# Performance work log

Measured on AMD Instinct MI355X. Metric: run time of the kernel, lower is better.

The kernel has to match this reference:

```python
import jax, jax.numpy as jnp
import numpy as np

N_NODES = 100000
N_EDGES = 1600000
NUM_GRAPHS = 128


def _gcn_layer(x, W, b, senders, receivers, n_node):
    # Linear transform first (cheaper: feature dim small)
    x = x @ W + b  # [N, out]
    ones = jnp.ones(senders.shape[0], dtype=x.dtype)
    deg_s = jax.ops.segment_sum(ones, senders, n_node)     # out-degree
    deg_r = jax.ops.segment_sum(ones, receivers, n_node)   # in-degree
    # symmetric normalization: D^-1/2 A D^-1/2
    x = x * jax.lax.rsqrt(jnp.maximum(deg_s, 1.0))[:, None]
    x = jax.ops.segment_sum(x[senders], receivers, n_node)  # gather-scatter aggregation
    x = x * jax.lax.rsqrt(jnp.maximum(deg_r, 1.0))[:, None]
    return x


def setup_inputs() -> dict:
    key = jax.random.key(0)
    ks = jax.random.split(key, 10)
    x = jax.random.normal(ks[0], (N_NODES, 9), dtype=jnp.float32)
    senders = jax.random.randint(ks[1], (N_EDGES,), 0, N_NODES)
    receivers = jax.random.randint(ks[2], (N_EDGES,), 0, N_NODES)
    batch = jnp.sort(jax.random.randint(ks[3], (N_NODES,), 0, NUM_GRAPHS))
    # learned params (Dense: W [in,out], b [out]) with LeCun-normal-ish scale
    def dense(k, din, dout):
        return jax.random.normal(k, (din, dout), dtype=jnp.float32) / np.sqrt(din)
    W1 = dense(ks[4], 9, 64)
    b1 = jnp.zeros((64,), jnp.float32)
    W2 = dense(ks[5], 64, 128)
    b2 = jnp.zeros((128,), jnp.float32)
    W3 = dense(ks[6], 128, 2)
    b3 = jnp.zeros((2,), jnp.float32)
    return {"x": x, "senders": senders, "receivers": receivers, "batch": batch,
            "num_graphs": NUM_GRAPHS, "W1": W1, "b1": b1, "W2": W2, "b2": b2,
            "W3": W3, "b3": b3}


def reference(x, senders, receivers, batch, num_graphs, W1, b1, W2, b2, W3, b3):
    n_node = x.shape[0]
    x = jax.nn.relu(_gcn_layer(x, W1, b1, senders, receivers, n_node))
    x = jax.nn.relu(_gcn_layer(x, W2, b2, senders, receivers, n_node))
    x = _gcn_layer(x, W3, b3, senders, receivers, n_node)
    # graph-level pooling
    return jax.ops.segment_sum(x, batch, num_graphs)
```

## Files before the change

kernel.cpp:

```cpp
#include <hip/hip_runtime.h>
#include <hip/hip_bf16.h>
#include <cstddef>

#define NBMAX 512
#define BCAP 5120
#define BKCHUNK 3200

typedef unsigned short bf16t;
typedef __attribute__((ext_vector_type(8))) short short8;
typedef __attribute__((ext_vector_type(4))) float f32x4;

static __device__ __forceinline__ float2 up2(unsigned u) {
    return make_float2(__uint_as_float(u << 16), __uint_as_float(u & 0xffff0000u));
}
static __device__ __forceinline__ bf16t f2bf(float f) {
    unsigned u = __float_as_uint(f);
    u += 0x7fffu + ((u >> 16) & 1u);
    return (bf16t)(u >> 16);
}
static __device__ __forceinline__ unsigned pk2(float a, float b) {
    return (unsigned)f2bf(a) | ((unsigned)f2bf(b) << 16);
}

__global__ void k_bucket(const int* __restrict__ S, const int* __restrict__ R,
                         unsigned* __restrict__ bufR, unsigned char* __restrict__ bufS,
                         int* __restrict__ gCntR, int* __restrict__ gCntS,
                         const float* __restrict__ W2, bf16t* __restrict__ W2f,
                         int nE, int nB) {
    __shared__ int histR[NBMAX], lstR[NBMAX], baseR[NBMAX];
    __shared__ int histS[NBMAX], lstS[NBMAX], baseS[NBMAX];
    __shared__ int sm[256];
    __shared__ unsigned sortedR[BKCHUNK];
    __shared__ unsigned short bOfR[BKCHUNK];
    __shared__ unsigned char sortedS[BKCHUNK];
    __shared__ unsigned short bOfS[BKCHUNK];
    int t = threadIdx.x;
    int nSort = gridDim.x - 4;
    if (blockIdx.x >= nSort) {
        int tt = (blockIdx.x - nSort) * blockDim.x + t;
        if (tt < 1024) {
            int nt = tt >> 7, kh = (tt >> 6) & 1, lane = tt & 63;
            int n = nt * 16 + (lane & 15);
            int k0 = kh * 32 + (lane >> 4) * 8;
            uint4 p;
            p.x = pk2(W2[(k0 + 0) * 128 + n], W2[(k0 + 1) * 128 + n]);
            p.y = pk2(W2[(k0 + 2) * 128 + n], W2[(k0 + 3) * 128 + n]);
            p.z = pk2(W2[(k0 + 4) * 128 + n], W2[(k0 + 5) * 128 + n]);
            p.w = pk2(W2[(k0 + 6) * 128 + n], W2[(k0 + 7) * 128 + n]);
            ((uint4*)W2f)[tt] = p;
        }
        return;
    }
    for (int i = t; i < NBMAX; i += 256) { histR[i] = 0; histS[i] = 0; }
    __syncthreads();
    int chunk = (nE + nSort - 1) / nSort;
    int e0 = blockIdx.x * chunk;
    int e1 = min(e0 + chunk, nE);
    for (int e = e0 + t; e < e1; e += 256) {
        atomicAdd(&histR[R[e] >> 8], 1);
        atomicAdd(&histS[S[e] >> 8], 1);
    }
    __syncthreads();
    {
        int c0 = histR[2 * t], c1 = histR[2 * t + 1];
        int ps = c0 + c1;
        sm[t] = ps;
        __syncthreads();
        for (int off = 1; off < 256; off <<= 1) {
            int y = (t >= off) ? sm[t - off] : 0;
            __syncthreads();
            sm[t] += y;
            __syncthreads();
        }
        int ex = sm[t] - ps;
        lstR[2 * t] = ex;
        lstR[2 * t + 1] = ex + c0;
    }
    __syncthreads();
    {
        int c0 = histS[2 * t], c1 = histS[2 * t + 1];
        int ps = c0 + c1;
        sm[t] = ps;
        __syncthreads();
        for (int off = 1; off < 256; off <<= 1) {
            int y = (t >= off) ? sm[t - off] : 0;
            __syncthreads();
            sm[t] += y;
            __syncthreads();
        }
        int ex = sm[t] - ps;
        lstS[2 * t] = ex;
        lstS[2 * t + 1] = ex + c0;
    }
    __syncthreads();
    for (int i = t; i < nB; i += 256) {
        int cR = histR[i];
        baseR[i] = cR ? atomicAdd(&gCntR[i], cR) : 0;
        int cS = histS[i];
        baseS[i] = cS ? atomicAdd(&gCntS[i], cS) : 0;
    }
    for (int i = t; i < NBMAX; i += 256) { histR[i] = 0; histS[i] = 0; }
    __syncthreads();
    for (int e = e0 + t; e < e1; e += 256) {
        int r = R[e], s = S[e];
        int br = r >> 8;
        int p = lstR[br] + atomicAdd(&histR[br], 1);
        sortedR[p] = ((unsigned)(r & 255) << 24) | (unsigned)s;
        bOfR[p] = (unsigned short)br;
        int bs = s >> 8;
        int p2 = lstS[bs] + atomicAdd(&histS[bs], 1);
        sortedS[p2] = (unsigned char)(s & 255);
        bOfS[p2] = (unsigned short)bs;
    }
    __syncthreads();
    int cnt = e1 - e0;
    for (int i = t; i < cnt; i += 256) {
        int b = bOfR[i];
        int slot = baseR[b] + (i - lstR[b]);
        if (slot < BCAP) bufR[(size_t)b * BCAP + slot] = sortedR[i];
        int b2 = bOfS[i];
        int slot2 = baseS[b2] + (i - lstS[b2]);
        if (slot2 < BCAP) bufS[(size_t)b2 * BCAP + slot2] = sortedS[i];
    }
}

__global__ void k_pass2(const unsigned* __restrict__ bufR, const unsigned char* __restrict__ bufS,
                        const int* __restrict__ gCntR, const int* __restrict__ gCntS,
                        const float* __restrict__ x,
                        int* __restrict__ csr, int* __restrict__ cur, int* __restrict__ degR,
                        float* __restrict__ inv_r, float* __restrict__ inv_s,
                        bf16t* __restrict__ xs, int nN, int nB) {
    __shared__ int hist[256], incl[256], curs[256], histS[256];
    __shared__ int sm[256];
    __shared__ int gex[NBMAX];
    int t = threadIdx.x;
    int b = blockIdx.x;
    {
        int c0 = (2 * t < nB) ? gCntR[2 * t] : 0;
        int c1 = (2 * t + 1 < nB) ? gCntR[2 * t + 1] : 0;
        int ps = c0 + c1;
        sm[t] = ps;
        __syncthreads();
        for (int off = 1; off < 256; off <<= 1) {
            int y = (t >= off) ? sm[t - off] : 0;
            __syncthreads();
            sm[t] += y;
            __syncthreads();
        }
        int ex = sm[t] - ps;
        gex[2 * t] = ex;
        gex[2 * t + 1] = ex + c0;
    }
    hist[t] = 0; curs[t] = 0; histS[t] = 0;
    __syncthreads();
    int gb = gex[b];
    int cnt = gCntR[b];
    const unsigned* buf = bufR + (size_t)b * BCAP;
    for (int i = t; i < cnt; i += 256) atomicAdd(&hist[buf[i] >> 24], 1);
    __syncthreads();
    int v = hist[t];
    sm[t] = v;
    __syncthreads();
    for (int off = 1; off < 256; off <<= 1) {
        int y = (t >= off) ? sm[t - off] : 0;
        __syncthreads();
        sm[t] += y;
        __syncthreads();
    }
    incl[t] = sm[t];
    __syncthreads();
    int n0 = b << 8;
    int n = n0 + t;
    if (n < nN) {
        degR[n] = v;
        cur[n] = gb + incl[t];
        inv_r[n] = rsqrtf(fmaxf((float)v, 1.f));
    }
    for (int i = t; i < cnt; i += 256) {
        unsigned p = buf[i];
        int rl = p >> 24;
        int s = p & 0xFFFFFF;
        int pos = gb + (incl[rl] - hist[rl]) + atomicAdd(&curs[rl], 1);
        csr[pos] = s;
    }
    int cntS = gCntS[b];
    const unsigned char* bufs = bufS + (size_t)b * BCAP;
    for (int i = t; i < cntS; i += 256) atomicAdd(&histS[bufs[i]], 1);
    __syncthreads();
    if (n < nN) {
        float is = rsqrtf(fmaxf((float)histS[t], 1.f));
        inv_s[n] = is;
        float w[9];
#pragma unroll
        for (int k = 0; k < 9; k++) w[k] = x[(size_t)n * 9 + k] * is;
        uint4 pa, pb;
        pa.x = pk2(w[0], w[1]); pa.y = pk2(w[2], w[3]);
        pa.z = pk2(w[4], w[5]); pa.w = pk2(w[6], w[7]);
        pb.x = pk2(w[8], is);   pb.y = 0; pb.z = 0; pb.w = 0;
        uint4* o = (uint4*)(xs + (size_t)n * 16);
        o[0] = pa;
        o[1] = pb;
    }
}

__global__ void k_h1f(const unsigned* __restrict__ xs32, const float* __restrict__ W1,
                      const float* __restrict__ b1,
                      const int* __restrict__ csr, const int* __restrict__ cur,
                      const int* __restrict__ degR, const float* __restrict__ inv_r,
                      const float* __restrict__ inv_s,
                      bf16t* __restrict__ h1s, float* __restrict__ warr, int nN) {
    __shared__ float Wl[9 * 64];
    __shared__ float bl[64];
    for (int i = threadIdx.x; i < 9 * 64; i += blockDim.x) Wl[i] = W1[i];
    if (threadIdx.x < 64) bl[threadIdx.x] = b1[threadIdx.x];
    __syncthreads();
    int lane = threadIdx.x & 63;
    int wave = threadIdx.x >> 6;
    int n = blockIdx.x * 16 + wave * 4 + (lane >> 4);
    int ql = lane & 15;
    int g = ql >> 2;
    int f2 = ql & 3;
    int nc = min(n, nN - 1);
    int deg = degR[nc];
    int st = cur[nc] - deg;
    float4 A0 = {0.f, 0.f, 0.f, 0.f}, A1 = A0, A2 = A0, A3 = A0;
    int i = 0;
    for (; i + 16 <= deg; i += 16) {
        int ea = csr[st + i + g];
        int eb = csr[st + i + 4 + g];
        int ec = csr[st + i + 8 + g];
        int ed = csr[st + i + 12 + g];
        uint2 u0 = *(const uint2*)(xs32 + (size_t)ea * 8 + f2 * 2);
        uint2 u1 = *(const uint2*)(xs32 + (size_t)eb * 8 + f2 * 2);
        uint2 u2 = *(const uint2*)(xs32 + (size_t)ec * 8 + f2 * 2);
        uint2 u3 = *(const uint2*)(xs32 + (size_t)ed * 8 + f2 * 2);
        float2 a = up2(u0.x), b = up2(u0.y);
        A0.x += a.x; A0.y += a.y; A0.z += b.x; A0.w += b.y;
        a = up2(u1.x); b = up2(u1.y);
        A1.x += a.x; A1.y += a.y; A1.z += b.x; A1.w += b.y;
        a = up2(u2.x); b = up2(u2.y);
        A2.x += a.x; A2.y += a.y; A2.z += b.x; A2.w += b.y;
        a = up2(u3.x); b = up2(u3.y);
        A3.x += a.x; A3.y += a.y; A3.z += b.x; A3.w += b.y;
    }
    for (; i + 4 <= deg; i += 4) {
        int ea = csr[st + i + g];
        uint2 u0 = *(const uint2*)(xs32 + (size_t)ea * 8 + f2 * 2);
        float2 a = up2(u0.x), b = up2(u0.y);
        A0.x += a.x; A0.y += a.y; A0.z += b.x; A0.w += b.y;
    }
    if (g < deg - i) {
        int ea = csr[st + i + g];
        uint2 u0 = *(const uint2*)(xs32 + (size_t)ea * 8 + f2 * 2);
        float2 a = up2(u0.x), b = up2(u0.y);
        A1.x += a.x; A1.y += a.y; A1.z += b.x; A1.w += b.y;
    }
    float4 vq = {(A0.x + A1.x) + (A2.x + A3.x), (A0.y + A1.y) + (A2.y + A3.y),
                 (A0.z + A1.z) + (A2.z + A3.z), (A0.w + A1.w) + (A2.w + A3.w)};
    vq.x += __shfl_xor(vq.x, 4); vq.y += __shfl_xor(vq.y, 4);
    vq.z += __shfl_xor(vq.z, 4); vq.w += __shfl_xor(vq.w, 4);
    vq.x += __shfl_xor(vq.x, 8); vq.y += __shfl_xor(vq.y, 8);
    vq.z += __shfl_xor(vq.z, 8); vq.w += __shfl_xor(vq.w, 8);
    int base = lane & 48;
    float xv[9];
    xv[0] = __shfl(vq.x, base + 0); xv[1] = __shfl(vq.y, base + 0);
    xv[2] = __shfl(vq.z, base + 0); xv[3] = __shfl(vq.w, base + 0);
    xv[4] = __shfl(vq.x, base + 1); xv[5] = __shfl(vq.y, base + 1);
    xv[6] = __shfl(vq.z, base + 1); xv[7] = __shfl(vq.w, base + 1);
    xv[8] = __shfl(vq.x, base + 2);
    float w = __shfl(vq.y, base + 2);
    float ir = inv_r[nc];
    float is = inv_s[nc];
    int c0 = ql * 4;
    float acc[4];
#pragma unroll
    for (int j = 0; j < 4; j++) acc[j] = w * bl[c0 + j];
#pragma unroll
    for (int k = 0; k < 9; k++) {
        float4 wv = *(const float4*)(Wl + k * 64 + c0);
        acc[0] += xv[k] * wv.x;
        acc[1] += xv[k] * wv.y;
        acc[2] += xv[k] * wv.z;
        acc[3] += xv[k] * wv.w;
    }
    if (n < nN) {
        float v0 = fmaxf(acc[0] * ir, 0.f) * is;
        float v1 = fmaxf(acc[1] * ir, 0.f) * is;
        float v2 = fmaxf(acc[2] * ir, 0.f) * is;
        float v3 = fmaxf(acc[3] * ir, 0.f) * is;
        uint2 pv;
        pv.x = pk2(v0, v1);
        pv.y = pk2(v2, v3);
        *(uint2*)(h1s + (size_t)n * 64 + c0) = pv;
        if (ql == 0) warr[n] = w;
    }
}

__global__ void __launch_bounds__(128, 8)
k_l2f(const unsigned* __restrict__ h32, const bf16t* __restrict__ W2f,
      const float* __restrict__ b2, const float* __restrict__ W3,
      const float* __restrict__ inv_r, const float* __restrict__ inv_s,
      const float* __restrict__ warr,
      const int* __restrict__ csr, const int* __restrict__ cur,
      const int* __restrict__ degR,
      float* __restrict__ t, float* __restrict__ dout, int outSize, int nN) {
    __shared__ float b2l[128];
    __shared__ float W3l[256];
    __shared__ unsigned zl[16 * 36];
    for (int i = threadIdx.x; i < 128; i += blockDim.x) b2l[i] = b2[i];
    for (int i = threadIdx.x; i < 256; i += blockDim.x) W3l[i] = W3[i];
    if (blockIdx.x == 0)
        for (int i = threadIdx.x; i < outSize; i += blockDim.x) dout[i] = 0.f;
    int lane = threadIdx.x & 63;
    int wave = threadIdx.x >> 6;
    int g3 = lane >> 3;
    int sub = lane & 7;
    int n0b = blockIdx.x * 16;
    {
        int roff = wave * 8 + g3;
        int nc = min(n0b + roff, nN - 1);
        int deg = degR[nc];
        int st = cur[nc] - deg;
        float a0 = 0.f, a1 = 0.f, a2 = 0.f, a3 = 0.f;
        float a4 = 0.f, a5 = 0.f, a6 = 0.f, a7 = 0.f;
        int i = 0;
        for (; i + 4 <= deg; i += 4) {
            int e0 = csr[st + i + 0];
            int e1 = csr[st + i + 1];
            int e2 = csr[st + i + 2];
            int e3 = csr[st + i + 3];
            uint4 u0 = *(const uint4*)(h32 + (size_t)e0 * 32 + sub * 4);
            uint4 u1 = *(const uint4*)(h32 + (size_t)e1 * 32 + sub * 4);
            uint4 u2 = *(const uint4*)(h32 + (size_t)e2 * 32 + sub * 4);
            uint4 u3 = *(const uint4*)(h32 + (size_t)e3 * 32 + sub * 4);
            float2 p;
            p = up2(u0.x); a0 += p.x; a1 += p.y;
            p = up2(u0.y); a2 += p.x; a3 += p.y;
            p = up2(u0.z); a4 += p.x; a5 += p.y;
            p = up2(u0.w); a6 += p.x; a7 += p.y;
            p = up2(u1.x); a0 += p.x; a1 += p.y;
            p = up2(u1.y); a2 += p.x; a3 += p.y;
            p = up2(u1.z); a4 += p.x; a5 += p.y;
            p = up2(u1.w); a6 += p.x; a7 += p.y;
            p = up2(u2.x); a0 += p.x; a1 += p.y;
            p = up2(u2.y); a2 += p.x; a3 += p.y;
            p = up2(u2.z); a4 += p.x; a5 += p.y;
            p = up2(u2.w); a6 += p.x; a7 += p.y;
            p = up2(u3.x); a0 += p.x; a1 += p.y;
            p = up2(u3.y); a2 += p.x; a3 += p.y;
            p = up2(u3.z); a4 += p.x; a5 += p.y;
            p = up2(u3.w); a6 += p.x; a7 += p.y;
        }
        for (; i < deg; i++) {
            int e0 = csr[st + i];
            uint4 u0 = *(const uint4*)(h32 + (size_t)e0 * 32 + sub * 4);
            float2 p;
            p = up2(u0.x); a0 += p.x; a1 += p.y;
            p = up2(u0.y); a2 += p.x; a3 += p.y;
            p = up2(u0.z); a4 += p.x; a5 += p.y;
            p = up2(u0.w); a6 += p.x; a7 += p.y;
        }
        uint4 pv;
        pv.x = pk2(a0, a1);
        pv.y = pk2(a2, a3);
        pv.z = pk2(a4, a5);
        pv.w = pk2(a6, a7);
        *(uint4*)(zl + roff * 36 + sub * 4) = pv;
    }
    __syncthreads();
    int m = lane & 15;
    int q = lane >> 4;
    short8 afr0 = *(const short8*)(zl + m * 36 + q * 4);
    short8 afr1 = *(const short8*)(zl + m * 36 + 16 + q * 4);
    float w4[4], ir4[4], is4[4];
#pragma unroll
    for (int reg = 0; reg < 4; reg++) {
        int nr = min(n0b + q * 4 + reg, nN - 1);
        w4[reg] = warr[nr];
        ir4[reg] = inv_r[nr];
        is4[reg] = inv_s[nr];
    }
    float p0[4] = {0.f, 0.f, 0.f, 0.f}, p1[4] = {0.f, 0.f, 0.f, 0.f};
#pragma unroll
    for (int nt = 0; nt < 8; nt++) {
        short8 b0 = *(const short8*)(W2f + ((size_t)(nt * 2 + 0) * 64 + lane) * 8);
        short8 b1 = *(const short8*)(W2f + ((size_t)(nt * 2 + 1) * 64 + lane) * 8);
        f32x4 acc = {0.f, 0.f, 0.f, 0.f};
        acc = __builtin_amdgcn_mfma_f32_16x16x32_bf16(afr0, b0, acc, 0, 0, 0);
        acc = __builtin_amdgcn_mfma_f32_16x16x32_bf16(afr1, b1, acc, 0, 0, 0);
        int col = nt * 16 + m;
        float bc = b2l[col];
        float w30 = W3l[col * 2 + 0];
        float w31 = W3l[col * 2 + 1];
#pragma unroll
        for (int reg = 0; reg < 4; reg++) {
            float h = fmaxf((acc[reg] + w4[reg] * bc) * ir4[reg], 0.f) * is4[reg];
            p0[reg] += h * w30;
            p1[reg] += h * w31;
        }
    }
#pragma unroll
    for (int mask = 1; mask < 16; mask <<= 1) {
#pragma unroll
        for (int reg = 0; reg < 4; reg++) {
            p0[reg] += __shfl_xor(p0[reg], mask);
            p1[reg] += __shfl_xor(p1[reg], mask);
        }
    }
    if (wave == 0 && m == 0) {
#pragma unroll
        for (int reg = 0; reg < 4; reg++) {
            int nr = n0b + q * 4 + reg;
            if (nr < nN) *(float2*)(t + (size_t)nr * 2) = make_float2(p0[reg], p1[reg]);
        }
    }
}

__global__ void k_poolg(const float* __restrict__ t, const float* __restrict__ inv_r,
                        const float* __restrict__ warr, const float* __restrict__ b3,
                        const int* __restrict__ csr, const int* __restrict__ cur,
                        const int* __restrict__ degR, const int* __restrict__ batch,
                        float* out, int nN, int outSize) {
    __shared__ float sm[256];
    for (int i = threadIdx.x; i < 256; i += blockDim.x) sm[i] = 0.f;
    __syncthreads();
    int tid = blockIdx.x * blockDim.x + threadIdx.x;
    int n = tid >> 3;
    int sub = tid & 7;
    if (n < nN) {
        int deg = degR[n];
        int st = cur[n] - deg;
        float a0 = 0.f, a1 = 0.f, c0 = 0.f, c1 = 0.f;
        int i = sub;
        for (; i + 8 < deg; i += 16) {
            int sa = csr[st + i], sb = csr[st + i + 8];
            float2 va = ((const float2*)t)[sa];
            float2 vb = ((const float2*)t)[sb];
            a0 += va.x; a1 += va.y;
            c0 += vb.x; c1 += vb.y;
        }
        for (; i < deg; i += 8) {
            float2 va = ((const float2*)t)[csr[st + i]];
            a0 += va.x; a1 += va.y;
        }
        float p0 = a0 + c0;
        float p1 = a1 + c1;
        p0 += __shfl_xor(p0, 1); p1 += __shfl_xor(p1, 1);
        p0 += __shfl_xor(p0, 2); p1 += __shfl_xor(p1, 2);
        p0 += __shfl_xor(p0, 4); p1 += __shfl_xor(p1, 4);
        if (sub == 0) {
            float ir = inv_r[n];
            float wb = warr[n] * ir;
            int g = batch[n];
            atomicAdd(&sm[2 * g + 0], p0 * ir + wb * b3[0]);
            atomicAdd(&sm[2 * g + 1], p1 * ir + wb * b3[1]);
        }
    }
    __syncthreads();
    for (int i = threadIdx.x; i < outSize; i += blockDim.x) {
        float v = sm[i];
        if (v != 0.f) atomicAdd(&out[i], v);
    }
}

extern "C" void kernel_launch(void* const* d_in, const int* in_sizes, int n_in,
                              void* d_out, int out_size, void* d_ws, size_t ws_size,
                              hipStream_t stream) {
    const float* x     = (const float*)d_in[0];
    const int*   S     = (const int*)d_in[1];
    const int*   R     = (const int*)d_in[2];
    const int*   batch = (const int*)d_in[3];
    const float* W1 = (const float*)d_in[5];
    const float* b1 = (const float*)d_in[6];
    const float* W2 = (const float*)d_in[7];
    const float* b2 = (const float*)d_in[8];
    const float* W3 = (const float*)d_in[9];
    const float* b3 = (const float*)d_in[10];

    int nN = in_sizes[0] / 9;
    int nE = in_sizes[1];
    int nB = (nN + 255) / 256;

    char* ws = (char*)d_ws;
    int*   cur   = (int*)ws;
    int*   degR  = cur + nN;
    float* inv_s = (float*)(degR + nN);
    float* inv_r = inv_s + nN;
    float* warr  = inv_r + nN;
    int*   gCntR = (int*)(warr + nN);
    int*   gCntS = gCntR + NBMAX;
    int*   csr   = gCntS + NBMAX;
    bf16t* xs    = (bf16t*)(csr + nE);
    bf16t* W2f   = xs + (size_t)nN * 16;
    char*  regA  = (char*)(W2f + 8192);
    unsigned*      bufR = (unsigned*)regA;
    unsigned char* bufS = (unsigned char*)(bufR + (size_t)NBMAX * BCAP);
    bf16t* h1s = (bf16t*)regA;
    float* t   = (float*)(regA + (size_t)NBMAX * BCAP * 5);

    const int B = 256;

    hipMemsetAsync(gCntR, 0, 2 * NBMAX * 4, stream);
    k_bucket<<<516, B, 0, stream>>>(S, R, bufR, bufS, gCntR, gCntS, W2, W2f, nE, nB);
    k_pass2<<<nB, B, 0, stream>>>(bufR, bufS, gCntR, gCntS, x, csr, cur, degR,
                                  inv_r, inv_s, xs, nN, nB);

    k_h1f<<<(nN + 15) / 16, B, 0, stream>>>((const unsigned*)xs, W1, b1, csr, cur, degR,
                                            inv_r, inv_s, h1s, warr, nN);

    k_l2f<<<(nN + 15) / 16, 128, 0, stream>>>((const unsigned*)h1s, W2f, b2, W3,
                                              inv_r, inv_s, warr, csr, cur, degR,
                                              t, (float*)d_out, out_size, nN);

    k_poolg<<<(nN * 8 + B - 1) / B, B, 0, stream>>>(t, inv_r, warr, b3, csr, cur, degR, batch,
                                                    (float*)d_out, nN, out_size);
}
```

Baseline: 214.4 us.

## Sort nodes by in-degree within blocks to balance gather work per wave

k_pass2 now builds a per-256-node permutation that counting-sorts nodes by in-degree. The aggregation kernels (h1f, l2f, poolg) process nodes through this permutation, so nodes handled by the same wave have similar degrees and loop trip counts diverge less. k_h1f also switches to 16-byte loads with 8 edges per step in place of 8-byte loads with 4 edges. The cost is an extra histogram and scan in pass2, one more indirection per node, and scattered output writes.

Result: slower. 229.0 us (+6.8%).

```diff
diff --git a/kernel.cpp b/kernel.cpp
--- a/kernel.cpp
+++ b/kernel.cpp
@@ -129,7 +129,7 @@
                         const float* __restrict__ x,
                         int* __restrict__ csr, int* __restrict__ cur, int* __restrict__ degR,
                         float* __restrict__ inv_r, float* __restrict__ inv_s,
-                        bf16t* __restrict__ xs, int nN, int nB) {
+                        bf16t* __restrict__ xs, int* __restrict__ perm, int nN, int nB) {
     __shared__ int hist[256], incl[256], curs[256], histS[256];
     __shared__ int sm[256];
     __shared__ int gex[NBMAX];
@@ -201,13 +201,37 @@
         o[0] = pa;
         o[1] = pb;
     }
+    __syncthreads();
+    hist[t] = 0;
+    curs[t] = 0;
+    __syncthreads();
+    int nInB = min(nN - n0, 256);
+    int dv = 0;
+    if (t < nInB) {
+        dv = min(v, 255);
+        atomicAdd(&hist[dv], 1);
+    }
+    __syncthreads();
+    int hv = hist[t];
+    sm[t] = hv;
+    __syncthreads();
+    for (int off = 1; off < 256; off <<= 1) {
+        int y = (t >= off) ? sm[t - off] : 0;
+        __syncthreads();
+        sm[t] += y;
+        __syncthreads();
+    }
+    if (t < nInB) {
+        int pos = (sm[dv] - hist[dv]) + atomicAdd(&curs[dv], 1);
+        perm[n0 + pos] = n;
+    }
 }
 
 __global__ void k_h1f(const unsigned* __restrict__ xs32, const float* __restrict__ W1,
                       const float* __restrict__ b1,
                       const int* __restrict__ csr, const int* __restrict__ cur,
                       const int* __restrict__ degR, const float* __restrict__ inv_r,
-                      const float* __restrict__ inv_s,
+                      const float* __restrict__ inv_s, const int* __restrict__ perm,
                       bf16t* __restrict__ h1s, float* __restrict__ warr, int nN) {
     __shared__ float Wl[9 * 64];
     __shared__ float bl[64];
@@ -216,65 +240,71 @@
     __syncthreads();
     int lane = threadIdx.x & 63;
     int wave = threadIdx.x >> 6;
-    int n = blockIdx.x * 16 + wave * 4 + (lane >> 4);
+    int j = blockIdx.x * 16 + wave * 4 + (lane >> 4);
+    int jc = min(j, nN - 1);
+    int nc = perm[jc];
     int ql = lane & 15;
-    int g = ql >> 2;
-    int f2 = ql & 3;
-    int nc = min(n, nN - 1);
+    int g = ql >> 1;
+    int f2 = ql & 1;
     int deg = degR[nc];
     int st = cur[nc] - deg;
-    float4 A0 = {0.f, 0.f, 0.f, 0.f}, A1 = A0, A2 = A0, A3 = A0;
+    float a0 = 0.f, a1 = 0.f, a2 = 0.f, a3 = 0.f;
+    float a4 = 0.f, a5 = 0.f, a6 = 0.f, a7 = 0.f;
     int i = 0;
     for (; i + 16 <= deg; i += 16) {
         int ea = csr[st + i + g];
-        int eb = csr[st + i + 4 + g];
-        int ec = csr[st + i + 8 + g];
-        int ed = csr[st + i + 12 + g];
-        uint2 u0 = *(const uint2*)(xs32 + (size_t)ea * 8 + f2 * 2);
-        uint2 u1 = *(const uint2*)(xs32 + (size_t)eb * 8 + f2 * 2);
-        uint2 u2 = *(const uint2*)(xs32 + (size_t)ec * 8 + f2 * 2);
-        uint2 u3 = *(const uint2*)(xs32 + (size_t)ed * 8 + f2 * 2);
-        float2 a = up2(u0.x), b = up2(u0.y);
-        A0.x += a.x; A0.y += a.y; A0.z += b.x; A0.w += b.y;
-        a = up2(u1.x); b = up2(u1.y);
-        A1.x += a.x; A1.y += a.y; A1.z += b.x; A1.w += b.y;
-        a = up2(u2.x); b = up2(u2.y);
-        A2.x += a.x; A2.y += a.y; A2.z += b.x; A2.w += b.y;
-        a = up2(u3.x); b = up2(u3.y);
-        A3.x += a.x; A3.y += a.y; A3.z += b.x; A3.w += b.y;
-    }
-    for (; i + 4 <= deg; i += 4) {
+        int eb = csr[st + i + 8 + g];
+        uint4 ua = *(const uint4*)(xs32 + (size_t)ea * 8 + f2 * 4);
+        uint4 ub = *(const uint4*)(xs32 + (size_t)eb * 8 + f2 * 4);
+        float2 p;
+        p = up2(ua.x); a0 += p.x; a1 += p.y;
+        p = up2(ua.y); a2 += p.x; a3 += p.y;
+        p = up2(ua.z); a4 += p.x; a5 += p.y;
+        p = up2(ua.w); a6 += p.x; a7 += p.y;
+        p = up2(ub.x); a0 += p.x; a1 += p.y;
+        p = up2(ub.y); a2 += p.x; a3 += p.y;
+        p = up2(ub.z); a4 += p.x; a5 += p.y;
+        p = up2(ub.w); a6 += p.x; a7 += p.y;
+    }
+    if (i + 8 <= deg) {
         int ea = csr[st + i + g];
-        uint2 u0 = *(const uint2*)(xs32 + (size_t)ea * 8 + f2 * 2);
-        float2 a = up2(u0.x), b = up2(u0.y);
-        A0.x += a.x; A0.y += a.y; A0.z += b.x; A0.w += b.y;
+        uint4 ua = *(const uint4*)(xs32 + (size_t)ea * 8 + f2 * 4);
+        float2 p;
+        p = up2(ua.x); a0 += p.x; a1 += p.y;
+        p = up2(ua.y); a2 += p.x; a3 += p.y;
+        p = up2(ua.z); a4 += p.x; a5 += p.y;
+        p = up2(ua.w); a6 += p.x; a7 += p.y;
+        i += 8;
     }
     if (g < deg - i) {
         int ea = csr[st + i + g];
-        uint2 u0 = *(const uint2*)(xs32 + (size_t)ea * 8 + f2 * 2);
-        float2 a = up2(u0.x), b = up2(u0.y);
-        A1.x += a.x; A1.y += a.y; A1.z += b.x; A1.w += b.y;
-    }
-    float4 vq = {(A0.x + A1.x) + (A2.x + A3.x), (A0.y + A1.y) + (A2.y + A3.y),
-                 (A0.z + A1.z) + (A2.z + A3.z), (A0.w + A1.w) + (A2.w + A3.w)};
-    vq.x += __shfl_xor(vq.x, 4); vq.y += __shfl_xor(vq.y, 4);
-    vq.z += __shfl_xor(vq.z, 4); vq.w += __shfl_xor(vq.w, 4);
-    vq.x += __shfl_xor(vq.x, 8); vq.y += __shfl_xor(vq.y, 8);
-    vq.z += __shfl_xor(vq.z, 8); vq.w += __shfl_xor(vq.w, 8);
+        uint4 ua = *(const uint4*)(xs32 + (size_t)ea * 8 + f2 * 4);
+        float2 p;
+        p = up2(ua.x); a0 += p.x; a1 += p.y;
+        p = up2(ua.y); a2 += p.x; a3 += p.y;
+        p = up2(ua.z); a4 += p.x; a5 += p.y;
+        p = up2(ua.w); a6 += p.x; a7 += p.y;
+    }
+    a0 += __shfl_xor(a0, 2); a1 += __shfl_xor(a1, 2); a2 += __shfl_xor(a2, 2); a3 += __shfl_xor(a3, 2);
+    a4 += __shfl_xor(a4, 2); a5 += __shfl_xor(a5, 2); a6 += __shfl_xor(a6, 2); a7 += __shfl_xor(a7, 2);
+    a0 += __shfl_xor(a0, 4); a1 += __shfl_xor(a1, 4); a2 += __shfl_xor(a2, 4); a3 += __shfl_xor(a3, 4);
+    a4 += __shfl_xor(a4, 4); a5 += __shfl_xor(a5, 4); a6 += __shfl_xor(a6, 4); a7 += __shfl_xor(a7, 4);
+    a0 += __shfl_xor(a0, 8); a1 += __shfl_xor(a1, 8); a2 += __shfl_xor(a2, 8); a3 += __shfl_xor(a3, 8);
+    a4 += __shfl_xor(a4, 8); a5 += __shfl_xor(a5, 8); a6 += __shfl_xor(a6, 8); a7 += __shfl_xor(a7, 8);
     int base = lane & 48;
     float xv[9];
-    xv[0] = __shfl(vq.x, base + 0); xv[1] = __shfl(vq.y, base + 0);
-    xv[2] = __shfl(vq.z, base + 0); xv[3] = __shfl(vq.w, base + 0);
-    xv[4] = __shfl(vq.x, base + 1); xv[5] = __shfl(vq.y, base + 1);
-    xv[6] = __shfl(vq.z, base + 1); xv[7] = __shfl(vq.w, base + 1);
-    xv[8] = __shfl(vq.x, base + 2);
-    float w = __shfl(vq.y, base + 2);
+    xv[0] = __shfl(a0, base); xv[1] = __shfl(a1, base);
+    xv[2] = __shfl(a2, base); xv[3] = __shfl(a3, base);
+    xv[4] = __shfl(a4, base); xv[5] = __shfl(a5, base);
+    xv[6] = __shfl(a6, base); xv[7] = __shfl(a7, base);
+    xv[8] = __shfl(a0, base + 1);
+    float w = __shfl(a1, base + 1);
     float ir = inv_r[nc];
     float is = inv_s[nc];
     int c0 = ql * 4;
     float acc[4];
 #pragma unroll
-    for (int j = 0; j < 4; j++) acc[j] = w * bl[c0 + j];
+    for (int jj = 0; jj < 4; jj++) acc[jj] = w * bl[c0 + jj];
 #pragma unroll
     for (int k = 0; k < 9; k++) {
         float4 wv = *(const float4*)(Wl + k * 64 + c0);
@@ -283,7 +313,7 @@
         acc[2] += xv[k] * wv.z;
         acc[3] += xv[k] * wv.w;
     }
-    if (n < nN) {
+    if (j < nN) {
         float v0 = fmaxf(acc[0] * ir, 0.f) * is;
         float v1 = fmaxf(acc[1] * ir, 0.f) * is;
         float v2 = fmaxf(acc[2] * ir, 0.f) * is;
@@ -291,8 +321,8 @@
         uint2 pv;
         pv.x = pk2(v0, v1);
         pv.y = pk2(v2, v3);
-        *(uint2*)(h1s + (size_t)n * 64 + c0) = pv;
-        if (ql == 0) warr[n] = w;
+        *(uint2*)(h1s + (size_t)nc * 64 + c0) = pv;
+        if (ql == 0) warr[nc] = w;
     }
 }
 
@@ -302,7 +332,7 @@
       const float* __restrict__ inv_r, const float* __restrict__ inv_s,
       const float* __restrict__ warr,
       const int* __restrict__ csr, const int* __restrict__ cur,
-      const int* __restrict__ degR,
+      const int* __restrict__ degR, const int* __restrict__ perm,
       float* __restrict__ t, float* __restrict__ dout, int outSize, int nN) {
     __shared__ float b2l[128];
     __shared__ float W3l[256];
@@ -318,7 +348,8 @@
     int n0b = blockIdx.x * 16;
     {
         int roff = wave * 8 + g3;
-        int nc = min(n0b + roff, nN - 1);
+        int jc = min(n0b + roff, nN - 1);
+        int nc = perm[jc];
         int deg = degR[nc];
         int st = cur[nc] - deg;
         float a0 = 0.f, a1 = 0.f, a2 = 0.f, a3 = 0.f;
@@ -373,9 +404,12 @@
     short8 afr0 = *(const short8*)(zl + m * 36 + q * 4);
     short8 afr1 = *(const short8*)(zl + m * 36 + 16 + q * 4);
     float w4[4], ir4[4], is4[4];
+    int nr4[4];
 #pragma unroll
     for (int reg = 0; reg < 4; reg++) {
-        int nr = min(n0b + q * 4 + reg, nN - 1);
+        int jr = min(n0b + q * 4 + reg, nN - 1);
+        int nr = perm[jr];
+        nr4[reg] = nr;
         w4[reg] = warr[nr];
         ir4[reg] = inv_r[nr];
         is4[reg] = inv_s[nr];
@@ -410,8 +444,8 @@
     if (wave == 0 && m == 0) {
 #pragma unroll
         for (int reg = 0; reg < 4; reg++) {
-            int nr = n0b + q * 4 + reg;
-            if (nr < nN) *(float2*)(t + (size_t)nr * 2) = make_float2(p0[reg], p1[reg]);
+            int jr = n0b + q * 4 + reg;
+            if (jr < nN) *(float2*)(t + (size_t)nr4[reg] * 2) = make_float2(p0[reg], p1[reg]);
         }
     }
 }
@@ -420,14 +454,16 @@
                         const float* __restrict__ warr, const float* __restrict__ b3,
                         const int* __restrict__ csr, const int* __restrict__ cur,
                         const int* __restrict__ degR, const int* __restrict__ batch,
+                        const int* __restrict__ perm,
                         float* out, int nN, int outSize) {
     __shared__ float sm[256];
     for (int i = threadIdx.x; i < 256; i += blockDim.x) sm[i] = 0.f;
     __syncthreads();
     int tid = blockIdx.x * blockDim.x + threadIdx.x;
-    int n = tid >> 3;
+    int j = tid >> 3;
     int sub = tid & 7;
-    if (n < nN) {
+    if (j < nN) {
+        int n = perm[j];
         int deg = degR[n];
         int st = cur[n] - deg;
         float a0 = 0.f, a1 = 0.f, c0 = 0.f, c1 = 0.f;
@@ -487,7 +523,8 @@
     float* inv_s = (float*)(degR + nN);
     float* inv_r = inv_s + nN;
     float* warr  = inv_r + nN;
-    int*   gCntR = (int*)(warr + nN);
+    int*   perm  = (int*)(warr + nN);
+    int*   gCntR = perm + nN;
     int*   gCntS = gCntR + NBMAX;
     int*   csr   = gCntS + NBMAX;
     bf16t* xs    = (bf16t*)(csr + nE);
@@ -503,15 +540,15 @@
     hipMemsetAsync(gCntR, 0, 2 * NBMAX * 4, stream);
     k_bucket<<<516, B, 0, stream>>>(S, R, bufR, bufS, gCntR, gCntS, W2, W2f, nE, nB);
     k_pass2<<<nB, B, 0, stream>>>(bufR, bufS, gCntR, gCntS, x, csr, cur, degR,
-                                  inv_r, inv_s, xs, nN, nB);
+                                  inv_r, inv_s, xs, perm, nN, nB);
 
     k_h1f<<<(nN + 15) / 16, B, 0, stream>>>((const unsigned*)xs, W1, b1, csr, cur, degR,
-                                            inv_r, inv_s, h1s, warr, nN);
+                                            inv_r, inv_s, perm, h1s, warr, nN);
 
     k_l2f<<<(nN + 15) / 16, 128, 0, stream>>>((const unsigned*)h1s, W2f, b2, W3,
-                                              inv_r, inv_s, warr, csr, cur, degR,
+                                              inv_r, inv_s, warr, csr, cur, degR, perm,
                                               t, (float*)d_out, out_size, nN);
 
     k_poolg<<<(nN * 8 + B - 1) / B, B, 0, stream>>>(t, inv_r, warr, b3, csr, cur, degR, batch,
-                                                    (float*)d_out, nN, out_size);
-}
+                                                    perm, (float*)d_out, nN, out_size);
+}
```
